# Optimization experiments

Measured on AMD Instinct MI355X. Metric: run time of the kernel, lower is better.

## Reference

```python
import jax, jax.numpy as jnp
import numpy as np

N_NODES = 50000
N_EDGES = 600000
HIDDEN = 128
NUM_FEAT = 3
NUM_CLASSES = 2
NUM_GRAPHS = 512


def setup_inputs() -> dict:
    key = jax.random.key(0)
    ks = jax.random.split(key, 12)
    x = jax.random.normal(ks[0], (N_NODES, NUM_FEAT), dtype=jnp.float32)
    edge_index = jax.random.randint(ks[1], (2, N_EDGES), 0, N_NODES, dtype=jnp.int64)
    batch = jnp.sort(jax.random.randint(ks[2], (N_NODES,), 0, NUM_GRAPHS, dtype=jnp.int64))

    def glorot(k, fan_in, fan_out):
        s = jnp.sqrt(6.0 / (fan_in + fan_out)).astype(jnp.float32)
        return jax.random.uniform(k, (fan_in, fan_out), jnp.float32, -s, s)

    return {
        "x": x,
        "W1": glorot(ks[3], NUM_FEAT, HIDDEN), "b1": jnp.zeros((HIDDEN,), jnp.float32),
        "W2": glorot(ks[4], HIDDEN, HIDDEN),  "b2": jnp.zeros((HIDDEN,), jnp.float32),
        "W3": glorot(ks[5], HIDDEN, HIDDEN),  "b3": jnp.zeros((HIDDEN,), jnp.float32),
        "W4": glorot(ks[6], HIDDEN, HIDDEN),  "b4": jnp.zeros((HIDDEN,), jnp.float32),
        "linW": glorot(ks[7], HIDDEN, NUM_CLASSES), "linb": jnp.zeros((NUM_CLASSES,), jnp.float32),
        "edge_index": edge_index,
        "batch": batch,
        "num_graphs": NUM_GRAPHS,
    }


def gcn_conv(x, W, b, src, dst, n_nodes):
    # PyG GCNConv: h = x W; out = D^-1/2 (A + I) D^-1/2 h + b
    h = x @ W                                    # [N, out]
    deg = jnp.zeros((n_nodes,), h.dtype).at[dst].add(1.0) + 1.0  # with self-loops
    dinv = jax.lax.rsqrt(deg)                    # [N]
    norm = dinv[src] * dinv[dst]                 # [E]
    msg = h[src] * norm[:, None]                 # gather + scale
    agg = jax.ops.segment_sum(msg, dst, num_segments=n_nodes)  # scatter-add
    agg = agg + h * (dinv * dinv)[:, None]       # self-loop contribution
    return agg + b


def reference(x, W1, b1, W2, b2, W3, b3, W4, b4, linW, linb, edge_index, batch, num_graphs):
    src, dst = edge_index[0], edge_index[1]
    n = x.shape[0]
    h = jax.nn.relu(gcn_conv(x, W1, b1, src, dst, n))
    h = jax.nn.relu(gcn_conv(h, W2, b2, src, dst, n))
    h = jax.nn.relu(gcn_conv(h, W3, b3, src, dst, n))
    h = gcn_conv(h, W4, b4, src, dst, n)
    # global_mean_pool over graphs
    sums = jax.ops.segment_sum(h, batch, num_segments=num_graphs)
    cnts = jax.ops.segment_sum(jnp.ones((n,), h.dtype), batch, num_segments=num_graphs)
    pooled = sums / jnp.maximum(cnts, 1.0)[:, None]
    # dropout is identity in eval mode
    return pooled @ linW + linb
```

## Files before the change

### kernel.cpp

```cpp
#include <hip/hip_runtime.h>
#include <hip/hip_bf16.h>

#define HID 128
#define NGRAPH 512

typedef __attribute__((ext_vector_type(8))) short short8;
typedef __attribute__((ext_vector_type(4))) float f32x4;

__device__ inline unsigned int f2bf(float f) {
    unsigned int u = __float_as_uint(f);
    return (u + 0x7FFFu + ((u >> 16) & 1u)) >> 16;
}
__device__ inline float bflo(unsigned int w) { return __uint_as_float(w << 16); }
__device__ inline float bfhi(unsigned int w) { return __uint_as_float(w & 0xFFFF0000u); }


__device__ inline void wcast_body(const float* __restrict__ W,
                                  unsigned short* __restrict__ Wt) {
    int t = threadIdx.x;
#pragma unroll
    for (int i = 0; i < 16; ++i) {
        int flat = i * 1024 + t;
        int n = flat >> 7, k = flat & 127;
        Wt[n * HID + k] = (unsigned short)f2bf(W[k * HID + n]);
    }
}

__global__ void k_setup1(int* __restrict__ deg, int n, int nzb,
                         const float* __restrict__ W4, const float* __restrict__ linW,
                         const float* __restrict__ b4, const float* __restrict__ linb,
                         float* __restrict__ W4p, float* __restrict__ b4p,
                         const float* __restrict__ W2, const float* __restrict__ W3,
                         unsigned short* __restrict__ Wt2, unsigned short* __restrict__ Wt3) {
    if ((int)blockIdx.x == nzb) {
        int idx = threadIdx.x;
        if (idx < 256) {
            int k = idx >> 1, c = idx & 1;
            float a = 0.0f;
            for (int j = 0; j < HID; ++j) a = fmaf(W4[k * HID + j], linW[j * 2 + c], a);
            W4p[idx] = a;
            if (idx < 2) {
                float b = 0.0f;
                for (int j = 0; j < HID; ++j) b = fmaf(b4[j], linW[j * 2 + idx], b);
                b4p[idx] = b + linb[idx];
            }
        }
        return;
    }
    if ((int)blockIdx.x == nzb + 1) { wcast_body(W2, Wt2); return; }
    if ((int)blockIdx.x == nzb + 2) { wcast_body(W3, Wt3); return; }
    int i = blockIdx.x * 1024 + threadIdx.x;
    if (i < n) deg[i] = 0;
}

__global__ void k_count(const int* __restrict__ ei, int* __restrict__ deg,
                        int* __restrict__ epos, int E) {
    int e = blockIdx.x * blockDim.x + threadIdx.x;
    if (e < E) epos[e] = atomicAdd(&deg[ei[E + e]], 1);
}

__global__ void k_scan2b(const int* __restrict__ deg, int* __restrict__ row_start,
                         float* __restrict__ dinv, const float* __restrict__ x,
                         float* __restrict__ Xs, int n, int nblocks) {
    __shared__ int rs[16];
    __shared__ int ws[16];
    __shared__ int s_off_sh;
    int lane = threadIdx.x & 63, wid = threadIdx.x >> 6;
    {
        int before = blockIdx.x * 1024;
        int p = 0;
        for (int i = threadIdx.x; i < before; i += 1024) p += deg[i];
#pragma unroll
        for (int off = 32; off; off >>= 1) p += __shfl_down(p, off);
        if (lane == 0) rs[wid] = p;
        __syncthreads();
        if (threadIdx.x == 0) {
            int s = 0;
#pragma unroll
            for (int w = 0; w < 16; ++w) s += rs[w];
            s_off_sh = s;
        }
        __syncthreads();
    }
    int i = blockIdx.x * 1024 + threadIdx.x;
    int v = (i < n) ? deg[i] : 0;
    if (i < n) {
        float dv = rsqrtf((float)v + 1.0f);
        dinv[i] = dv;
        float4 r;
        r.x = x[i * 3 + 0] * dv;
        r.y = x[i * 3 + 1] * dv;
        r.z = x[i * 3 + 2] * dv;
        r.w = 0.0f;
        *(float4*)&Xs[i * 4] = r;
    }
    int xx = v;
#pragma unroll
    for (int off = 1; off < 64; off <<= 1) {
        int t = __shfl_up(xx, off);
        if (lane >= off) xx += t;
    }
    if (lane == 63) ws[wid] = xx;
    __syncthreads();
    int wo = 0;
    for (int w = 0; w < wid; ++w) wo += ws[w];
    int excl = s_off_sh + wo + xx - v;
    if (i < n) row_start[i] = excl;
    if ((int)blockIdx.x == nblocks - 1 && threadIdx.x == 0) {
        int ct = 0;
#pragma unroll
        for (int w = 0; w < 16; ++w) ct += ws[w];
        row_start[n] = s_off_sh + ct;
    }
}

__global__ void k_fill(const int* __restrict__ ei, const int* __restrict__ row_start,
                       const int* __restrict__ epos, int* __restrict__ src_sorted, int E) {
    int e = blockIdx.x * blockDim.x + threadIdx.x;
    if (e < E) {
        int s = ei[e];
        int d = ei[E + e];
        src_sorted[row_start[d] + epos[e]] = s;
    }
}

__global__ __launch_bounds__(256) void k_l1g2(const float* __restrict__ Xs,
                                              const int* __restrict__ row_start,
                                              const int* __restrict__ src_sorted,
                                              const float* __restrict__ dinv,
                                              const float* __restrict__ W1,
                                              const float* __restrict__ b1,
                                              const unsigned short* __restrict__ Wtg,
                                              unsigned short* __restrict__ Hout, int n) {
    __shared__ unsigned short Wt[HID * HID];
    __shared__ unsigned short AT[64 * HID];
    __shared__ float xs[64][4];

    {
        int nrow = threadIdx.x >> 1, s = threadIdx.x & 1;
        int xr = (nrow & 7) << 3;
#pragma unroll
        for (int i = 0; i < 8; ++i) {
            int b16 = s * 64 + i * 8;
            *(uint4*)&Wt[nrow * HID + (b16 ^ xr)] = *(const uint4*)&Wtg[nrow * HID + b16];
        }
    }
    {
        int grp = threadIdx.x >> 2, sub = threadIdx.x & 3;
        int v = blockIdx.x * 64 + grp;
        float a0 = 0.f, a1 = 0.f, a2 = 0.f;
        if (v < n) {
            int e0 = row_start[v], e1 = row_start[v + 1];
            for (int e = e0 + sub; e < e1; e += 4) {
                int s2 = src_sorted[e];
                float4 xv = *(const float4*)&Xs[s2 * 4];
                a0 += xv.x; a1 += xv.y; a2 += xv.z;
            }
        }
        a0 += __shfl_xor(a0, 2); a0 += __shfl_xor(a0, 1);
        a1 += __shfl_xor(a1, 2); a1 += __shfl_xor(a1, 1);
        a2 += __shfl_xor(a2, 2); a2 += __shfl_xor(a2, 1);
        if (sub == 0) {
            if (v < n) {
                float dv = dinv[v];
                float4 xv = *(const float4*)&Xs[v * 4];
                xs[grp][0] = (a0 + xv.x) * dv;
                xs[grp][1] = (a1 + xv.y) * dv;
                xs[grp][2] = (a2 + xv.z) * dv;
            } else {
                xs[grp][0] = 0.f; xs[grp][1] = 0.f; xs[grp][2] = 0.f;
            }
        }
    }
    __syncthreads();
    {
#pragma unroll
        for (int i = 0; i < 16; ++i) {
            int flat = i * 256 + threadIdx.x;
            int row = flat >> 6, cp = flat & 63;
            float x0 = xs[row][0], x1 = xs[row][1], x2 = xs[row][2];
            int c0 = cp * 2, c1 = c0 + 1;
            float r0 = fmaf(x0, W1[c0], fmaf(x1, W1[HID + c0], fmaf(x2, W1[2 * HID + c0], b1[c0])));
            float r1 = fmaf(x0, W1[c1], fmaf(x1, W1[HID + c1], fmaf(x2, W1[2 * HID + c1], b1[c1])));
            unsigned int w = f2bf(fmaxf(r0, 0.f)) | (f2bf(fmaxf(r1, 0.f)) << 16);
            int soff = (c0 & 7) | ((((c0 >> 3)) ^ (row & 7)) << 3);
            *(unsigned int*)&AT[row * HID + soff] = w;
        }
    }
    __syncthreads();
    int w    = threadIdx.x >> 6;
    int lane = threadIdx.x & 63;
    int g    = lane >> 4;
    int mr   = lane & 15;
    size_t row0 = (size_t)blockIdx.x * 64;
    int arow = w * 16 + mr;
    int axr = (arow & 7) << 3;

    short8 a[4];
#pragma unroll
    for (int ks = 0; ks < 4; ++ks)
        a[ks] = *(const short8*)&AT[arow * HID + ((ks * 32 + g * 8) ^ axr)];

    f32x4 acc[8];
#pragma unroll
    for (int nt = 0; nt < 8; ++nt) acc[nt] = (f32x4){0.f, 0.f, 0.f, 0.f};

#pragma unroll
    for (int nt = 0; nt < 8; ++nt) {
        int nrow = nt * 16 + mr;
        int xr = (nrow & 7) << 3;
        short8 b[4];
#pragma unroll
        for (int ks = 0; ks < 4; ++ks)
            b[ks] = *(const short8*)&Wt[nrow * HID + ((ks * 32 + g * 8) ^ xr)];
#pragma unroll
        for (int ks = 0; ks < 4; ++ks)
            acc[nt] = __builtin_amdgcn_mfma_f32_16x16x32_bf16(a[ks], b[ks], acc[nt], 0, 0, 0);
    }
    __syncthreads();
    {
        int rrb = w * 16 + g * 4;
#pragma unroll
        for (int j = 0; j < 4; ++j) {
            int rr = rrb + j;
            float dv = dinv[row0 + rr];
#pragma unroll
            for (int nt = 0; nt < 8; ++nt) {
                int col = nt * 16 + mr;
                int idx = rr * HID + ((col & 7) | ((((col >> 3)) ^ (rr & 7)) << 3));
                AT[idx] = (unsigned short)f2bf(acc[nt][j] * dv);
            }
        }
    }
    __syncthreads();
    {
        int rr = threadIdx.x >> 2, s = threadIdx.x & 3;
        int xr = (rr & 7) << 3;
#pragma unroll
        for (int i = 0; i < 4; ++i) {
            int b16 = s * 32 + i * 8;
            uint4 v = *(const uint4*)&AT[rr * HID + (b16 ^ xr)];
            *(uint4*)&Hout[(row0 + rr) * HID + b16] = v;
        }
    }
}

__global__ __launch_bounds__(256) void k_gemm_mfma(const unsigned short* __restrict__ X,
                                                   const unsigned short* __restrict__ Wtg,
                                                   const float* __restrict__ dinv,
                                                   unsigned short* __restrict__ Hout) {
    __shared__ unsigned short Wt[HID * HID];
    {
        int nrow = threadIdx.x >> 1, s = threadIdx.x & 1;
        int xr = (nrow & 7) << 3;
#pragma unroll
        for (int i = 0; i < 8; ++i) {
            int b16 = s * 64 + i * 8;
            uint4 src = *(const uint4*)&Wtg[nrow * HID + b16];
            *(uint4*)&Wt[nrow * HID + (b16 ^ xr)] = src;
        }
    }
    __syncthreads();

    int w    = threadIdx.x >> 6;
    int lane = threadIdx.x & 63;
    int g    = lane >> 4;
    int mr   = lane & 15;
    size_t row0 = (size_t)blockIdx.x * 64;
    size_t arow = row0 + w * 16 + mr;

    short8 a[4];
#pragma unroll
    for (int ks = 0; ks < 4; ++ks)
        a[ks] = *(const short8*)&X[arow * HID + ks * 32 + g * 8];

    f32x4 acc[8];
#pragma unroll
    for (int nt = 0; nt < 8; ++nt) acc[nt] = (f32x4){0.f, 0.f, 0.f, 0.f};

#pragma unroll
    for (int nt = 0; nt < 8; ++nt) {
        int nrow = nt * 16 + mr;
        int xr = (nrow & 7) << 3;
        short8 b[4];
#pragma unroll
        for (int ks = 0; ks < 4; ++ks)
            b[ks] = *(const short8*)&Wt[nrow * HID + ((ks * 32 + g * 8) ^ xr)];
#pragma unroll
        for (int ks = 0; ks < 4; ++ks)
            acc[nt] = __builtin_amdgcn_mfma_f32_16x16x32_bf16(a[ks], b[ks], acc[nt], 0, 0, 0);
    }

    __syncthreads();
    {
        int rrb = w * 16 + g * 4;
#pragma unroll
        for (int j = 0; j < 4; ++j) {
            int rr = rrb + j;
            float dv = dinv[row0 + rr];
#pragma unroll
            for (int nt = 0; nt < 8; ++nt) {
                int col = nt * 16 + mr;
                int idx = rr * HID + ((col & 7) | ((((col >> 3)) ^ (rr & 7)) << 3));
                Wt[idx] = (unsigned short)f2bf(acc[nt][j] * dv);
            }
        }
    }
    __syncthreads();
    {
        int rr = threadIdx.x >> 2, s = threadIdx.x & 3;
        int xr = (rr & 7) << 3;
#pragma unroll
        for (int i = 0; i < 4; ++i) {
            int b16 = s * 32 + i * 8;
            uint4 v = *(const uint4*)&Wt[rr * HID + (b16 ^ xr)];
            *(uint4*)&Hout[(row0 + rr) * HID + b16] = v;
        }
    }
}

__global__ __launch_bounds__(256) void k_gather(const unsigned short* __restrict__ Hs,
                                                const int* __restrict__ row_start,
                                                const int* __restrict__ src_sorted,
                                                const float* __restrict__ dinv,
                                                const float* __restrict__ bias,
                                                unsigned short* __restrict__ Aout, int n) {
    int wid  = (blockIdx.x * blockDim.x + threadIdx.x) >> 6;
    int lane = threadIdx.x & 63;
    int q = lane >> 4, ql = lane & 15;
    int v0 = wid * 4;
    if (v0 >= n) return;
    int v  = v0 + q;
    bool real = (v < n);
    int vc = real ? v : v0;
    int e0 = row_start[vc], e1 = row_start[vc + 1];
    int deg = e1 - e0;
    int idx0 = (ql < deg) ? src_sorted[e0 + ql] : vc;
    int idx1 = (16 + ql < deg) ? src_sorted[e0 + 16 + ql] : vc;
    float4 accA = make_float4(0.f, 0.f, 0.f, 0.f);
    float4 accB = make_float4(0.f, 0.f, 0.f, 0.f);
    {
        uint4 h[16];
#pragma unroll
        for (int j = 0; j < 16; ++j) {
            int sj = __shfl(idx0, (q << 4) | j);
            uint4 hv = make_uint4(0u, 0u, 0u, 0u);
            if (j < deg) hv = *(const uint4*)&Hs[(size_t)sj * HID + ql * 8];
            h[j] = hv;
        }
#pragma unroll
        for (int j = 0; j < 16; ++j) {
            accA.x += bflo(h[j].x); accA.y += bfhi(h[j].x);
            accA.z += bflo(h[j].y); accA.w += bfhi(h[j].y);
            accB.x += bflo(h[j].z); accB.y += bfhi(h[j].z);
            accB.z += bflo(h[j].w); accB.w += bfhi(h[j].w);
        }
    }
    if (deg > 16) {
        uint4 h[16];
#pragma unroll
        for (int j = 0; j < 16; ++j) {
            int sj = __shfl(idx1, (q << 4) | j);
            uint4 hv = make_uint4(0u, 0u, 0u, 0u);
            if (16 + j < deg) hv = *(const uint4*)&Hs[(size_t)sj * HID + ql * 8];
            h[j] = hv;
        }
#pragma unroll
        for (int j = 0; j < 16; ++j) {
            accA.x += bflo(h[j].x); accA.y += bfhi(h[j].x);
            accA.z += bflo(h[j].y); accA.w += bfhi(h[j].y);
            accB.x += bflo(h[j].z); accB.y += bfhi(h[j].z);
            accB.z += bflo(h[j].w); accB.w += bfhi(h[j].w);
        }
    }
    for (int e = e0 + 32; e < e1; ++e) {
        int sj = src_sorted[e];
        uint4 h = *(const uint4*)&Hs[(size_t)sj * HID + ql * 8];
        accA.x += bflo(h.x); accA.y += bfhi(h.x);
        accA.z += bflo(h.y); accA.w += bfhi(h.y);
        accB.x += bflo(h.z); accB.y += bfhi(h.z);
        accB.z += bflo(h.w); accB.w += bfhi(h.w);
    }
    float dv = dinv[vc];
    uint4 sv = *(const uint4*)&Hs[(size_t)vc * HID + ql * 8];
    float4 bbA = *(const float4*)&bias[ql * 8 + 0];
    float4 bbB = *(const float4*)&bias[ql * 8 + 4];
    float o0 = fmaxf(fmaf(accA.x + bflo(sv.x), dv, bbA.x), 0.f);
    float o1 = fmaxf(fmaf(accA.y + bfhi(sv.x), dv, bbA.y), 0.f);
    float o2 = fmaxf(fmaf(accA.z + bflo(sv.y), dv, bbA.z), 0.f);
    float o3 = fmaxf(fmaf(accA.w + bfhi(sv.y), dv, bbA.w), 0.f);
    float o4 = fmaxf(fmaf(accB.x + bflo(sv.z), dv, bbB.x), 0.f);
    float o5 = fmaxf(fmaf(accB.y + bfhi(sv.z), dv, bbB.y), 0.f);
    float o6 = fmaxf(fmaf(accB.z + bflo(sv.w), dv, bbB.z), 0.f);
    float o7 = fmaxf(fmaf(accB.w + bfhi(sv.w), dv, bbB.w), 0.f);
    if (real) {
        uint4 o;
        o.x = f2bf(o0) | (f2bf(o1) << 16);
        o.y = f2bf(o2) | (f2bf(o3) << 16);
        o.z = f2bf(o4) | (f2bf(o5) << 16);
        o.w = f2bf(o6) | (f2bf(o7) << 16);
        *(uint4*)&Aout[(size_t)v * HID + ql * 8] = o;
    }
}

__global__ __launch_bounds__(256) void k_gather_proj(const unsigned short* __restrict__ Hs,
                                                     const int* __restrict__ row_start,
                                                     const int* __restrict__ src_sorted,
                                                     const float* __restrict__ dinv,
                                                     const float* __restrict__ bias,
                                                     const float* __restrict__ W4p,
                                                     float* __restrict__ P3s, int n) {
    int wid  = (blockIdx.x * blockDim.x + threadIdx.x) >> 6;
    int lane = threadIdx.x & 63;
    int q = lane >> 4, ql = lane & 15;
    int v0 = wid * 4;
    if (v0 >= n) return;
    int v  = v0 + q;
    bool real = (v < n);
    int vc = real ? v : v0;
    int e0 = row_start[vc], e1 = row_start[vc + 1];
    int deg = e1 - e0;
    int idx0 = (ql < deg) ? src_sorted[e0 + ql] : vc;
    int idx1 = (16 + ql < deg) ? src_sorted[e0 + 16 + ql] : vc;
    float4 accA = make_float4(0.f, 0.f, 0.f, 0.f);
    float4 accB = make_float4(0.f, 0.f, 0.f, 0.f);
    {
        uint4 h[16];
#pragma unroll
        for (int j = 0; j < 16; ++j) {
            int sj = __shfl(idx0, (q << 4) | j);
            uint4 hv = make_uint4(0u, 0u, 0u, 0u);
            if (j < deg) hv = *(const uint4*)&Hs[(size_t)sj * HID + ql * 8];
            h[j] = hv;
        }
#pragma unroll
        for (int j = 0; j < 16; ++j) {
            accA.x += bflo(h[j].x); accA.y += bfhi(h[j].x);
            accA.z += bflo(h[j].y); accA.w += bfhi(h[j].y);
            accB.x += bflo(h[j].z); accB.y += bfhi(h[j].z);
            accB.z += bflo(h[j].w); accB.w += bfhi(h[j].w);
        }
    }
    if (deg > 16) {
        uint4 h[16];
#pragma unroll
        for (int j = 0; j < 16; ++j) {
            int sj = __shfl(idx1, (q << 4) | j);
            uint4 hv = make_uint4(0u, 0u, 0u, 0u);
            if (16 + j < deg) hv = *(const uint4*)&Hs[(size_t)sj * HID + ql * 8];
            h[j] = hv;
        }
#pragma unroll
        for (int j = 0; j < 16; ++j) {
            accA.x += bflo(h[j].x); accA.y += bfhi(h[j].x);
            accA.z += bflo(h[j].y); accA.w += bfhi(h[j].y);
            accB.x += bflo(h[j].z); accB.y += bfhi(h[j].z);
            accB.z += bflo(h[j].w); accB.w += bfhi(h[j].w);
        }
    }
    for (int e = e0 + 32; e < e1; ++e) {
        int sj = src_sorted[e];
        uint4 h = *(const uint4*)&Hs[(size_t)sj * HID + ql * 8];
        accA.x += bflo(h.x); accA.y += bfhi(h.x);
        accA.z += bflo(h.y); accA.w += bfhi(h.y);
        accB.x += bflo(h.z); accB.y += bfhi(h.z);
        accB.z += bflo(h.w); accB.w += bfhi(h.w);
    }
    float dv = dinv[vc];
    uint4 sv = *(const uint4*)&Hs[(size_t)vc * HID + ql * 8];
    float4 bbA = *(const float4*)&bias[ql * 8 + 0];
    float4 bbB = *(const float4*)&bias[ql * 8 + 4];
    float o0 = fmaxf(fmaf(accA.x + bflo(sv.x), dv, bbA.x), 0.f);
    float o1 = fmaxf(fmaf(accA.y + bfhi(sv.x), dv, bbA.y), 0.f);
    float o2 = fmaxf(fmaf(accA.z + bflo(sv.y), dv, bbA.z), 0.f);
    float o3 = fmaxf(fmaf(accA.w + bfhi(sv.y), dv, bbA.w), 0.f);
    float o4 = fmaxf(fmaf(accB.x + bflo(sv.z), dv, bbB.x), 0.f);
    float o5 = fmaxf(fmaf(accB.y + bfhi(sv.z), dv, bbB.y), 0.f);
    float o6 = fmaxf(fmaf(accB.z + bflo(sv.w), dv, bbB.z), 0.f);
    float o7 = fmaxf(fmaf(accB.w + bfhi(sv.w), dv, bbB.w), 0.f);
    float4 w0 = *(const float4*)&W4p[ql * 16 + 0];
    float4 w1 = *(const float4*)&W4p[ql * 16 + 4];
    float4 w2 = *(const float4*)&W4p[ql * 16 + 8];
    float4 w3 = *(const float4*)&W4p[ql * 16 + 12];
    float p0 = o0 * w0.x + o1 * w0.z + o2 * w1.x + o3 * w1.z
             + o4 * w2.x + o5 * w2.z + o6 * w3.x + o7 * w3.z;
    float p1 = o0 * w0.y + o1 * w0.w + o2 * w1.y + o3 * w1.w
             + o4 * w2.y + o5 * w2.w + o6 * w3.y + o7 * w3.w;
#pragma unroll
    for (int off = 8; off; off >>= 1) {
        p0 += __shfl_xor(p0, off);
        p1 += __shfl_xor(p1, off);
    }
    if (ql == 0 && real) *(float2*)&P3s[v * 2] = make_float2(p0 * dv, p1 * dv);
}

__global__ __launch_bounds__(256) void k_tail(const float* __restrict__ P3s,
                                              const int* __restrict__ row_start,
                                              const int* __restrict__ src_sorted,
                                              const float* __restrict__ dinv,
                                              const int* __restrict__ batch,
                                              const float* __restrict__ b4p,
                                              float* __restrict__ out, int n) {
    int g = blockIdx.x;
    int lo = 0, hi = n;
    while (lo < hi) { int m = (lo + hi) >> 1; if (batch[m] < g) lo = m + 1; else hi = m; }
    int start = lo;
    hi = n;
    while (lo < hi) { int m = (lo + hi) >> 1; if (batch[m] < g + 1) lo = m + 1; else hi = m; }
    int end = lo;

    int grp = threadIdx.x >> 3, sub = threadIdx.x & 7;
    float gx = 0.f, gy = 0.f;
    for (int v = start + grp; v < end; v += 32) {
        float ax = 0.f, ay = 0.f;
        int e0 = row_start[v], e1 = row_start[v + 1];
        for (int e = e0 + sub; e < e1; e += 8) {
            int s = src_sorted[e];
            float2 ps = *(const float2*)&P3s[s * 2];
            ax += ps.x;
            ay += ps.y;
        }
#pragma unroll
        for (int off = 4; off; off >>= 1) {
            ax += __shfl_down(ax, off);
            ay += __shfl_down(ay, off);
        }
        if (sub == 0) {
            float dv = dinv[v];
            float2 pv = *(const float2*)&P3s[v * 2];
            gx += (ax + pv.x) * dv;
            gy += (ay + pv.y) * dv;
        }
    }
    __shared__ float red[64];
    if (sub == 0) { red[grp] = gx; red[grp + 32] = gy; }
    __syncthreads();
    if (threadIdx.x < 64) {
        float sx = (threadIdx.x < 32) ? red[threadIdx.x] : 0.f;
        float sy = (threadIdx.x < 32) ? red[threadIdx.x + 32] : 0.f;
#pragma unroll
        for (int off = 16; off; off >>= 1) {
            sx += __shfl_down(sx, off);
            sy += __shfl_down(sy, off);
        }
        if (threadIdx.x == 0) {
            float inv = 1.0f / fmaxf((float)(end - start), 1.0f);
            out[g * 2 + 0] = sx * inv + b4p[0];
            out[g * 2 + 1] = sy * inv + b4p[1];
        }
    }
}


extern "C" void kernel_launch(void* const* d_in, const int* in_sizes, int n_in,
                              void* d_out, int out_size, void* d_ws, size_t ws_size,
                              hipStream_t stream) {
    const float* x    = (const float*)d_in[0];
    const float* W1   = (const float*)d_in[1];
    const float* b1   = (const float*)d_in[2];
    const float* W2   = (const float*)d_in[3];
    const float* b2   = (const float*)d_in[4];
    const float* W3   = (const float*)d_in[5];
    const float* b3   = (const float*)d_in[6];
    const float* W4   = (const float*)d_in[7];
    const float* b4   = (const float*)d_in[8];
    const float* linW = (const float*)d_in[9];
    const float* linb = (const float*)d_in[10];
    const int*   ei   = (const int*)d_in[11];
    const int*   batch= (const int*)d_in[12];
    float* out        = (float*)d_out;

    const int N = in_sizes[0] / 3;
    const int E = in_sizes[11] / 2;
    const int NPAD = ((N + 127) / 128) * 128;
    const int NB1024 = (N + 1023) / 1024;

    float* ws = (float*)d_ws;
    float* dinv       = ws;
    int*   deg_i      = (int*)(ws + 50176);
    int*   row_start  = (int*)(ws + 100352);
    int*   epos       = (int*)(ws + 150784);
    float* W4p        = ws + 750912;
    float* b4p        = ws + 751168;
    int*   src_sorted = (int*)(ws + 751232);
    float* P3s        = ws + 1351296;
    float* Xs         = ws + 1451648;
    unsigned short* Hbuf16 = (unsigned short*)(ws + 1652352);
    unsigned short* Act16  = (unsigned short*)(ws + 1652352 + (size_t)NPAD * 64);
    unsigned short* Wt2g   = (unsigned short*)(ws + 1652352 + 2 * (size_t)NPAD * 64);
    unsigned short* Wt3g   = Wt2g + HID * HID;

    const int B = 256;

    k_setup1<<<NB1024 + 3, 1024, 0, stream>>>(deg_i, N, NB1024, W4, linW, b4, linb,
                                              W4p, b4p, W2, W3, Wt2g, Wt3g);
    k_count<<<(E + B - 1) / B, B, 0, stream>>>(ei, deg_i, epos, E);
    k_scan2b<<<NB1024, 1024, 0, stream>>>(deg_i, row_start, dinv, x, Xs, N, NB1024);
    k_fill<<<(E + B - 1) / B, B, 0, stream>>>(ei, row_start, epos, src_sorted, E);

    const int gatherBlocks = (N + 15) / 16;
    const int gemmBlocks   = NPAD / 64;

    k_l1g2<<<gemmBlocks, B, 0, stream>>>(Xs, row_start, src_sorted, dinv, W1, b1,
                                         Wt2g, Hbuf16, N);
    k_gather<<<gatherBlocks, B, 0, stream>>>(Hbuf16, row_start, src_sorted, dinv, b2, Act16, N);
    k_gemm_mfma<<<gemmBlocks, B, 0, stream>>>(Act16, Wt3g, dinv, Hbuf16);
    k_gather_proj<<<gatherBlocks, B, 0, stream>>>(Hbuf16, row_start, src_sorted, dinv, b3, W4p, P3s, N);
    k_tail<<<NGRAPH, B, 0, stream>>>(P3s, row_start, src_sorted, dinv, batch, b4p, out, N);
}
```

Before: 162.2 us.

## Fuse layer-2 neighbor gather with layer-3 MFMA GEMM into one kernel

Merges the gather/aggregate kernel and the following bf16 MFMA GEMM into one kernel. Each 64-row block gathers its aggregated activations into shared memory (swizzled), then runs the MFMA projection directly from LDS. The output goes to a separate buffer to avoid overwriting the gather source. This drops one kernel launch and the global round trip of the intermediate activation, at the cost of more LDS per block (48KB), which limits occupancy for the latency-bound gather phase.

```diff
diff --git a/kernel.cpp b/kernel.cpp
--- a/kernel.cpp
+++ b/kernel.cpp
@@ -245,161 +245,156 @@
     }
 }
 
-__global__ __launch_bounds__(256) void k_gemm_mfma(const unsigned short* __restrict__ X,
-                                                   const unsigned short* __restrict__ Wtg,
-                                                   const float* __restrict__ dinv,
-                                                   unsigned short* __restrict__ Hout) {
+__global__ __launch_bounds__(256) void k_gagm(const unsigned short* __restrict__ Hs,
+                                              const int* __restrict__ row_start,
+                                              const int* __restrict__ src_sorted,
+                                              const float* __restrict__ dinv,
+                                              const float* __restrict__ bias,
+                                              const unsigned short* __restrict__ Wtg,
+                                              unsigned short* __restrict__ Hout, int n) {
     __shared__ unsigned short Wt[HID * HID];
+    __shared__ unsigned short AT[64 * HID];
+
     {
         int nrow = threadIdx.x >> 1, s = threadIdx.x & 1;
         int xr = (nrow & 7) << 3;
 #pragma unroll
         for (int i = 0; i < 8; ++i) {
             int b16 = s * 64 + i * 8;
-            uint4 src = *(const uint4*)&Wtg[nrow * HID + b16];
-            *(uint4*)&Wt[nrow * HID + (b16 ^ xr)] = src;
-        }
-    }
-    __syncthreads();
+            *(uint4*)&Wt[nrow * HID + (b16 ^ xr)] = *(const uint4*)&Wtg[nrow * HID + b16];
+        }
+    }
 
     int w    = threadIdx.x >> 6;
     int lane = threadIdx.x & 63;
-    int g    = lane >> 4;
-    int mr   = lane & 15;
+    int q = lane >> 4, ql = lane & 15;
     size_t row0 = (size_t)blockIdx.x * 64;
-    size_t arow = row0 + w * 16 + mr;
-
-    short8 a[4];
-#pragma unroll
-    for (int ks = 0; ks < 4; ++ks)
-        a[ks] = *(const short8*)&X[arow * HID + ks * 32 + g * 8];
-
-    f32x4 acc[8];
-#pragma unroll
-    for (int nt = 0; nt < 8; ++nt) acc[nt] = (f32x4){0.f, 0.f, 0.f, 0.f};
-
-#pragma unroll
-    for (int nt = 0; nt < 8; ++nt) {
-        int nrow = nt * 16 + mr;
-        int xr = (nrow & 7) << 3;
-        short8 b[4];
-#pragma unroll
-        for (int ks = 0; ks < 4; ++ks)
-            b[ks] = *(const short8*)&Wt[nrow * HID + ((ks * 32 + g * 8) ^ xr)];
-#pragma unroll
-        for (int ks = 0; ks < 4; ++ks)
-            acc[nt] = __builtin_amdgcn_mfma_f32_16x16x32_bf16(a[ks], b[ks], acc[nt], 0, 0, 0);
-    }
-
-    __syncthreads();
-    {
-        int rrb = w * 16 + g * 4;
-#pragma unroll
-        for (int j = 0; j < 4; ++j) {
-            int rr = rrb + j;
-            float dv = dinv[row0 + rr];
-#pragma unroll
-            for (int nt = 0; nt < 8; ++nt) {
-                int col = nt * 16 + mr;
-                int idx = rr * HID + ((col & 7) | ((((col >> 3)) ^ (rr & 7)) << 3));
-                Wt[idx] = (unsigned short)f2bf(acc[nt][j] * dv);
-            }
-        }
-    }
-    __syncthreads();
-    {
-        int rr = threadIdx.x >> 2, s = threadIdx.x & 3;
-        int xr = (rr & 7) << 3;
-#pragma unroll
-        for (int i = 0; i < 4; ++i) {
-            int b16 = s * 32 + i * 8;
-            uint4 v = *(const uint4*)&Wt[rr * HID + (b16 ^ xr)];
-            *(uint4*)&Hout[(row0 + rr) * HID + b16] = v;
-        }
-    }
-}
-
-__global__ __launch_bounds__(256) void k_gather(const unsigned short* __restrict__ Hs,
-                                                const int* __restrict__ row_start,
-                                                const int* __restrict__ src_sorted,
-                                                const float* __restrict__ dinv,
-                                                const float* __restrict__ bias,
-                                                unsigned short* __restrict__ Aout, int n) {
-    int wid  = (blockIdx.x * blockDim.x + threadIdx.x) >> 6;
-    int lane = threadIdx.x & 63;
-    int q = lane >> 4, ql = lane & 15;
-    int v0 = wid * 4;
-    if (v0 >= n) return;
-    int v  = v0 + q;
-    bool real = (v < n);
-    int vc = real ? v : v0;
-    int e0 = row_start[vc], e1 = row_start[vc + 1];
-    int deg = e1 - e0;
-    int idx0 = (ql < deg) ? src_sorted[e0 + ql] : vc;
-    int idx1 = (16 + ql < deg) ? src_sorted[e0 + 16 + ql] : vc;
-    float4 accA = make_float4(0.f, 0.f, 0.f, 0.f);
-    float4 accB = make_float4(0.f, 0.f, 0.f, 0.f);
-    {
-        uint4 h[16];
-#pragma unroll
-        for (int j = 0; j < 16; ++j) {
-            int sj = __shfl(idx0, (q << 4) | j);
-            uint4 hv = make_uint4(0u, 0u, 0u, 0u);
-            if (j < deg) hv = *(const uint4*)&Hs[(size_t)sj * HID + ql * 8];
-            h[j] = hv;
-        }
-#pragma unroll
-        for (int j = 0; j < 16; ++j) {
-            accA.x += bflo(h[j].x); accA.y += bfhi(h[j].x);
-            accA.z += bflo(h[j].y); accA.w += bfhi(h[j].y);
-            accB.x += bflo(h[j].z); accB.y += bfhi(h[j].z);
-            accB.z += bflo(h[j].w); accB.w += bfhi(h[j].w);
-        }
-    }
-    if (deg > 16) {
-        uint4 h[16];
-#pragma unroll
-        for (int j = 0; j < 16; ++j) {
-            int sj = __shfl(idx1, (q << 4) | j);
-            uint4 hv = make_uint4(0u, 0u, 0u, 0u);
-            if (16 + j < deg) hv = *(const uint4*)&Hs[(size_t)sj * HID + ql * 8];
-            h[j] = hv;
-        }
-#pragma unroll
-        for (int j = 0; j < 16; ++j) {
-            accA.x += bflo(h[j].x); accA.y += bfhi(h[j].x);
-            accA.z += bflo(h[j].y); accA.w += bfhi(h[j].y);
-            accB.x += bflo(h[j].z); accB.y += bfhi(h[j].z);
-            accB.z += bflo(h[j].w); accB.w += bfhi(h[j].w);
-        }
-    }
-    for (int e = e0 + 32; e < e1; ++e) {
-        int sj = src_sorted[e];
-        uint4 h = *(const uint4*)&Hs[(size_t)sj * HID + ql * 8];
-        accA.x += bflo(h.x); accA.y += bfhi(h.x);
-        accA.z += bflo(h.y); accA.w += bfhi(h.y);
-        accB.x += bflo(h.z); accB.y += bfhi(h.z);
-        accB.z += bflo(h.w); accB.w += bfhi(h.w);
-    }
-    float dv = dinv[vc];
-    uint4 sv = *(const uint4*)&Hs[(size_t)vc * HID + ql * 8];
-    float4 bbA = *(const float4*)&bias[ql * 8 + 0];
-    float4 bbB = *(const float4*)&bias[ql * 8 + 4];
-    float o0 = fmaxf(fmaf(accA.x + bflo(sv.x), dv, bbA.x), 0.f);
-    float o1 = fmaxf(fmaf(accA.y + bfhi(sv.x), dv, bbA.y), 0.f);
-    float o2 = fmaxf(fmaf(accA.z + bflo(sv.y), dv, bbA.z), 0.f);
-    float o3 = fmaxf(fmaf(accA.w + bfhi(sv.y), dv, bbA.w), 0.f);
-    float o4 = fmaxf(fmaf(accB.x + bflo(sv.z), dv, bbB.x), 0.f);
-    float o5 = fmaxf(fmaf(accB.y + bfhi(sv.z), dv, bbB.y), 0.f);
-    float o6 = fmaxf(fmaf(accB.z + bflo(sv.w), dv, bbB.z), 0.f);
-    float o7 = fmaxf(fmaf(accB.w + bfhi(sv.w), dv, bbB.w), 0.f);
-    if (real) {
+
+    for (int pass = 0; pass < 4; ++pass) {
+        int r = pass * 16 + w * 4 + q;
+        int v = (int)row0 + r;
+        int vc = (v < n) ? v : (n - 1);
+        int e0 = row_start[vc], e1 = row_start[vc + 1];
+        int deg = e1 - e0;
+        int idx0 = (ql < deg) ? src_sorted[e0 + ql] : vc;
+        int idx1 = (16 + ql < deg) ? src_sorted[e0 + 16 + ql] : vc;
+        float4 accA = make_float4(0.f, 0.f, 0.f, 0.f);
+        float4 accB = make_float4(0.f, 0.f, 0.f, 0.f);
+        {
+            uint4 h[16];
+#pragma unroll
+            for (int j = 0; j < 16; ++j) {
+                int sj = __shfl(idx0, (q << 4) | j);
+                uint4 hv = make_uint4(0u, 0u, 0u, 0u);
+                if (j < deg) hv = *(const uint4*)&Hs[(size_t)sj * HID + ql * 8];
+                h[j] = hv;
+            }
+#pragma unroll
+            for (int j = 0; j < 16; ++j) {
+                accA.x += bflo(h[j].x); accA.y += bfhi(h[j].x);
+                accA.z += bflo(h[j].y); accA.w += bfhi(h[j].y);
+                accB.x += bflo(h[j].z); accB.y += bfhi(h[j].z);
+                accB.z += bflo(h[j].w); accB.w += bfhi(h[j].w);
+            }
+        }
+        if (deg > 16) {
+            uint4 h[16];
+#pragma unroll
+            for (int j = 0; j < 16; ++j) {
+                int sj = __shfl(idx1, (q << 4) | j);
+                uint4 hv = make_uint4(0u, 0u, 0u, 0u);
+                if (16 + j < deg) hv = *(const uint4*)&Hs[(size_t)sj * HID + ql * 8];
+                h[j] = hv;
+            }
+#pragma unroll
+            for (int j = 0; j < 16; ++j) {
+                accA.x += bflo(h[j].x); accA.y += bfhi(h[j].x);
+                accA.z += bflo(h[j].y); accA.w += bfhi(h[j].y);
+                accB.x += bflo(h[j].z); accB.y += bfhi(h[j].z);
+                accB.z += bflo(h[j].w); accB.w += bfhi(h[j].w);
+            }
+        }
+        for (int e = e0 + 32; e < e1; ++e) {
+            int sj = src_sorted[e];
+            uint4 h = *(const uint4*)&Hs[(size_t)sj * HID + ql * 8];
+            accA.x += bflo(h.x); accA.y += bfhi(h.x);
+            accA.z += bflo(h.y); accA.w += bfhi(h.y);
+            accB.x += bflo(h.z); accB.y += bfhi(h.z);
+            accB.z += bflo(h.w); accB.w += bfhi(h.w);
+        }
+        float dv = dinv[vc];
+        uint4 sv = *(const uint4*)&Hs[(size_t)vc * HID + ql * 8];
+        float4 bbA = *(const float4*)&bias[ql * 8 + 0];
+        float4 bbB = *(const float4*)&bias[ql * 8 + 4];
+        float o0 = fmaxf(fmaf(accA.x + bflo(sv.x), dv, bbA.x), 0.f);
+        float o1 = fmaxf(fmaf(accA.y + bfhi(sv.x), dv, bbA.y), 0.f);
+        float o2 = fmaxf(fmaf(accA.z + bflo(sv.y), dv, bbA.z), 0.f);
+        float o3 = fmaxf(fmaf(accA.w + bfhi(sv.y), dv, bbA.w), 0.f);
+        float o4 = fmaxf(fmaf(accB.x + bflo(sv.z), dv, bbB.x), 0.f);
+        float o5 = fmaxf(fmaf(accB.y + bfhi(sv.z), dv, bbB.y), 0.f);
+        float o6 = fmaxf(fmaf(accB.z + bflo(sv.w), dv, bbB.z), 0.f);
+        float o7 = fmaxf(fmaf(accB.w + bfhi(sv.w), dv, bbB.w), 0.f);
         uint4 o;
         o.x = f2bf(o0) | (f2bf(o1) << 16);
         o.y = f2bf(o2) | (f2bf(o3) << 16);
         o.z = f2bf(o4) | (f2bf(o5) << 16);
         o.w = f2bf(o6) | (f2bf(o7) << 16);
-        *(uint4*)&Aout[(size_t)v * HID + ql * 8] = o;
+        int chunk = ql ^ (r & 7);
+        *(uint4*)&AT[r * HID + chunk * 8] = o;
+    }
+    __syncthreads();
+
+    int g  = lane >> 4;
+    int mr = lane & 15;
+    int arow = w * 16 + mr;
+    int axr = (arow & 7) << 3;
+
+    short8 a[4];
+#pragma unroll
+    for (int ks = 0; ks < 4; ++ks)
+        a[ks] = *(const short8*)&AT[arow * HID + ((ks * 32 + g * 8) ^ axr)];
+
+    f32x4 acc[8];
+#pragma unroll
+    for (int nt = 0; nt < 8; ++nt) acc[nt] = (f32x4){0.f, 0.f, 0.f, 0.f};
+
+#pragma unroll
+    for (int nt = 0; nt < 8; ++nt) {
+        int nrow = nt * 16 + mr;
+        int xr = (nrow & 7) << 3;
+        short8 b[4];
+#pragma unroll
+        for (int ks = 0; ks < 4; ++ks)
+            b[ks] = *(const short8*)&Wt[nrow * HID + ((ks * 32 + g * 8) ^ xr)];
+#pragma unroll
+        for (int ks = 0; ks < 4; ++ks)
+            acc[nt] = __builtin_amdgcn_mfma_f32_16x16x32_bf16(a[ks], b[ks], acc[nt], 0, 0, 0);
+    }
+    __syncthreads();
+    {
+        int rrb = w * 16 + g * 4;
+#pragma unroll
+        for (int j = 0; j < 4; ++j) {
+            int rr = rrb + j;
+            float dv = dinv[row0 + rr];
+#pragma unroll
+            for (int nt = 0; nt < 8; ++nt) {
+                int col = nt * 16 + mr;
+                int idx = rr * HID + ((col & 7) | ((((col >> 3)) ^ (rr & 7)) << 3));
+                AT[idx] = (unsigned short)f2bf(acc[nt][j] * dv);
+            }
+        }
+    }
+    __syncthreads();
+    {
+        int rr = threadIdx.x >> 2, s = threadIdx.x & 3;
+        int xr = (rr & 7) << 3;
+#pragma unroll
+        for (int i = 0; i < 4; ++i) {
+            int b16 = s * 32 + i * 8;
+            uint4 v = *(const uint4*)&AT[rr * HID + (b16 ^ xr)];
+            *(uint4*)&Hout[(row0 + rr) * HID + b16] = v;
+        }
     }
 }
 
@@ -586,7 +581,7 @@
     float* P3s        = ws + 1351296;
     float* Xs         = ws + 1451648;
     unsigned short* Hbuf16 = (unsigned short*)(ws + 1652352);
-    unsigned short* Act16  = (unsigned short*)(ws + 1652352 + (size_t)NPAD * 64);
+    unsigned short* H3buf  = (unsigned short*)(ws + 1652352 + (size_t)NPAD * 64);
     unsigned short* Wt2g   = (unsigned short*)(ws + 1652352 + 2 * (size_t)NPAD * 64);
     unsigned short* Wt3g   = Wt2g + HID * HID;
 
@@ -603,8 +598,8 @@
 
     k_l1g2<<<gemmBlocks, B, 0, stream>>>(Xs, row_start, src_sorted, dinv, W1, b1,
                                          Wt2g, Hbuf16, N);
-    k_gather<<<gatherBlocks, B, 0, stream>>>(Hbuf16, row_start, src_sorted, dinv, b2, Act16, N);
-    k_gemm_mfma<<<gemmBlocks, B, 0, stream>>>(Act16, Wt3g, dinv, Hbuf16);
-    k_gather_proj<<<gatherBlocks, B, 0, stream>>>(Hbuf16, row_start, src_sorted, dinv, b3, W4p, P3s, N);
+    k_gagm<<<gemmBlocks, B, 0, stream>>>(Hbuf16, row_start, src_sorted, dinv, b2,
+                                         Wt3g, H3buf, N);
+    k_gather_proj<<<gatherBlocks, B, 0, stream>>>(H3buf, row_start, src_sorted, dinv, b3, W4p, P3s, N);
     k_tail<<<NGRAPH, B, 0, stream>>>(P3s, row_start, src_sorted, dinv, batch, b4p, out, N);
 }
```

Result: faster. 157.1 us (-3.1%).
